# Optimization experiments

Hardware: AMD Instinct MI355X
Metric: run time of the kernel (lower is better)

The kernel has to match this reference:

```python
import jax, jax.numpy as jnp
import numpy as np

NEG_SLOPE = 0.2   # PyG GATConv default leaky_relu slope
L2_EPS = 1e-12    # F.normalize eps


def setup_inputs() -> dict:
    key = jax.random.key(0)
    ks = jax.random.split(key, 10)
    N, E, d = 100000, 600000, 128
    s = 1.0 / np.sqrt(d)
    return {
        "x": jax.random.normal(ks[0], (N, d), jnp.float32),
        "edge_index": jax.random.randint(ks[1], (2, E), 0, N, jnp.int64),
        "W_gat": jax.random.normal(ks[2], (d, d), jnp.float32) * s,
        "att_src": jax.random.normal(ks[3], (d,), jnp.float32) * s,
        "att_dst": jax.random.normal(ks[4], (d,), jnp.float32) * s,
        "b_gat": jax.random.normal(ks[5], (d,), jnp.float32) * s,
        "W_l": jax.random.normal(ks[6], (d, d), jnp.float32) * s,
        "b_l": jax.random.normal(ks[7], (d,), jnp.float32) * s,
        "W_r": jax.random.normal(ks[8], (d, d), jnp.float32) * s,
    }


def reference(x, edge_index, W_gat, att_src, att_dst, b_gat, W_l, b_l, W_r):
    N = x.shape[0]
    src0, dst0 = edge_index[0], edge_index[1]

    # ---- GATConv (heads=1), add_self_loops=True, dropout skipped (eval) ----
    loop = jnp.arange(N, dtype=edge_index.dtype)
    src = jnp.concatenate([src0, loop])
    dst = jnp.concatenate([dst0, loop])

    h = x @ W_gat                           # [N, d]
    a_src = h @ att_src                     # [N]
    a_dst = h @ att_dst                     # [N]
    e = jax.nn.leaky_relu(a_src[src] + a_dst[dst], NEG_SLOPE)  # [E+N]
    # segment softmax over edges sharing the same target node
    m = jax.ops.segment_max(e, dst, num_segments=N)
    p = jnp.exp(e - m[dst])
    z = jax.ops.segment_sum(p, dst, num_segments=N)
    alpha = p / z[dst]
    h_gat = jax.ops.segment_sum(h[src] * alpha[:, None], dst, num_segments=N) + b_gat

    # ---- SAGEConv((x, x_target), edge_index), mean aggr, normalize=True ----
    agg = jax.ops.segment_sum(h_gat[src0], dst0, num_segments=N)   # [N, d]
    cnt = jax.ops.segment_sum(jnp.ones_like(src0, dtype=h_gat.dtype), dst0, num_segments=N)
    mean = agg / jnp.maximum(cnt, 1.0)[:, None]
    out = mean @ W_l + b_l + h_gat @ W_r    # x_target = h_gat[:N]
    # F.normalize(out, p=2, dim=-1)
    norm = jnp.sqrt(jnp.sum(out * out, axis=-1, keepdims=True))
    out = out / jnp.maximum(norm, L2_EPS)
    return out
```

## Files before the change

kernel.cpp:

```cpp
#include <hip/hip_runtime.h>
#include <hip/hip_bf16.h>

#define D 128
#define NEG_SLOPE 0.2f
#define SCAN_BS 512
#define RT 4
#define RTH 2

typedef __attribute__((ext_vector_type(8))) short short8;
typedef __attribute__((ext_vector_type(4))) short short4v;
typedef __attribute__((ext_vector_type(4))) float f32x4;

__device__ __forceinline__ float group_max16(float v) {
#pragma unroll
    for (int m = 8; m >= 1; m >>= 1) v = fmaxf(v, __shfl_xor(v, m));
    return v;
}
__device__ __forceinline__ float group_sum16(float v) {
#pragma unroll
    for (int m = 8; m >= 1; m >>= 1) v += __shfl_xor(v, m);
    return v;
}

__device__ __forceinline__ unsigned short f2bfu(float f) {
    __hip_bfloat16 h = __float2bfloat16(f);
    return *reinterpret_cast<unsigned short*>(&h);
}

__device__ __forceinline__ float bf2f(unsigned short u) {
    return __uint_as_float(((unsigned)u) << 16);
}

__device__ __forceinline__ short8 load_bf8(const float* p) {
    float4 p0 = *(const float4*)p;
    float4 p1 = *(const float4*)(p + 4);
    short8 r;
    r[0] = (short)f2bfu(p0.x); r[1] = (short)f2bfu(p0.y);
    r[2] = (short)f2bfu(p0.z); r[3] = (short)f2bfu(p0.w);
    r[4] = (short)f2bfu(p1.x); r[5] = (short)f2bfu(p1.y);
    r[6] = (short)f2bfu(p1.z); r[7] = (short)f2bfu(p1.w);
    return r;
}

__global__ void k_wt(const float* __restrict__ Wg, const float* __restrict__ Wl,
                     const float* __restrict__ Wr, short* __restrict__ WgT,
                     short* __restrict__ WlT, short* __restrict__ WrT) {
    int i = blockIdx.x * blockDim.x + threadIdx.x;
    int m = i >> 14;
    int r = (i >> 7) & 127;
    int c = i & 127;
    const float* src = (m == 0) ? Wg : (m == 1) ? Wl : Wr;
    short* dst = (m == 0) ? WgT : (m == 1) ? WlT : WrT;
    dst[r * D + c] = (short)f2bfu(src[c * D + r]);
}

__global__ void k_hist(const int* __restrict__ ei, int* __restrict__ cnt, int E) {
    int i = blockIdx.x * blockDim.x + threadIdx.x;
    if (i < E) atomicAdd(&cnt[ei[E + i]], 1);
}

__global__ void k_scan_block(const int* __restrict__ cnt, int* __restrict__ incl,
                             int* __restrict__ btot, int N) {
    __shared__ int s[SCAN_BS];
    int t = threadIdx.x, i = blockIdx.x * SCAN_BS + t;
    int v = (i < N) ? cnt[i] : 0;
    s[t] = v;
    __syncthreads();
    for (int d = 1; d < SCAN_BS; d <<= 1) {
        int u = (t >= d) ? s[t - d] : 0;
        __syncthreads();
        s[t] += u;
        __syncthreads();
    }
    if (i < N) incl[i] = s[t];
    if (t == SCAN_BS - 1) btot[blockIdx.x] = s[t];
}

__global__ void k_scan_tot(int* __restrict__ btot, int nb) {
    __shared__ int s[1024];
    int t = threadIdx.x;
    int v = (t < nb) ? btot[t] : 0;
    s[t] = v;
    __syncthreads();
    for (int d = 1; d < 1024; d <<= 1) {
        int u = (t >= d) ? s[t - d] : 0;
        __syncthreads();
        s[t] += u;
        __syncthreads();
    }
    if (t < nb) btot[t] = s[t] - v;
}

__global__ void k_scan_add(const int* __restrict__ cnt, int* __restrict__ off,
                           const int* __restrict__ btot, int N) {
    int i = blockIdx.x * blockDim.x + threadIdx.x;
    if (i < N) off[i] = off[i] + btot[i / SCAN_BS] - cnt[i];
}

__global__ void k_bucket(const int* __restrict__ ei, const int* __restrict__ off,
                         int* __restrict__ fill, int* __restrict__ csr, int E) {
    int i = blockIdx.x * blockDim.x + threadIdx.x;
    if (i < E) {
        int dt = ei[E + i];
        int p = off[dt] + atomicAdd(&fill[dt], 1);
        csr[p] = ei[i];
    }
}

__global__ void __launch_bounds__(256, 1)
k_gemm_h(const float* __restrict__ x, const short* __restrict__ WgT,
         const float* __restrict__ att_src, const float* __restrict__ att_dst,
         unsigned short* __restrict__ h_bf, float* __restrict__ a_src,
         float* __restrict__ a_dst, int N) {
    __shared__ short lds_w[D * D];
    const int tid = threadIdx.x;
#pragma unroll
    for (int i = 0; i < 8; ++i) {
        int go = (i * 256 + tid) * 16;
        int so = go ^ (((go >> 8) & 7) << 4);
        *(short8*)((char*)lds_w + so) = *(const short8*)((const char*)WgT + go);
    }
    __syncthreads();

    const int lane = tid & 63;
    const int wave = tid >> 6;
    const int lrow = lane & 15, lgrp = lane >> 4;
    const int swz = (lrow & 7) << 4;
    const int base = blockIdx.x * (64 * RTH) + wave * (16 * RTH);

    short8 ax[RTH][4];
    int rows[RTH];
    bool okr[RTH];
#pragma unroll
    for (int t = 0; t < RTH; ++t) {
        rows[t] = base + t * 16 + lrow;
        okr[t] = (rows[t] < N);
        const float* xr = x + (size_t)rows[t] * D + lgrp * 8;
#pragma unroll
        for (int kt = 0; kt < 4; ++kt) {
            if (okr[t]) ax[t][kt] = load_bf8(xr + kt * 32);
            else { short8 zf; for (int j = 0; j < 8; ++j) zf[j] = 0; ax[t][kt] = zf; }
        }
    }

    float ps[RTH], pd[RTH];
#pragma unroll
    for (int t = 0; t < RTH; ++t) { ps[t] = 0.f; pd[t] = 0.f; }

#pragma unroll
    for (int f = 0; f < 8; ++f) {
        short8 wgf[4];
#pragma unroll
        for (int kt = 0; kt < 4; ++kt) {
            int byte = (f * 16 + lrow) * 256 + kt * 64 + lgrp * 16;
            wgf[kt] = *(const short8*)((const char*)lds_w + (byte ^ swz));
        }
        const int cb = f * 16 + lgrp * 4;
        float as[4], adv[4];
#pragma unroll
        for (int j = 0; j < 4; ++j) { as[j] = att_src[cb + j]; adv[j] = att_dst[cb + j]; }
#pragma unroll
        for (int t = 0; t < RTH; ++t) {
            f32x4 a = (f32x4){0.f, 0.f, 0.f, 0.f};
#pragma unroll
            for (int kt = 0; kt < 4; ++kt)
                a = __builtin_amdgcn_mfma_f32_16x16x32_bf16(wgf[kt], ax[t][kt], a, 0, 0, 0);
            short4v hv;
#pragma unroll
            for (int j = 0; j < 4; ++j) {
                float v = a[j];
                hv[j] = (short)f2bfu(v);
                ps[t] += v * as[j];
                pd[t] += v * adv[j];
            }
            if (okr[t]) *(short4v*)(h_bf + (size_t)rows[t] * D + cb) = hv;
        }
    }
#pragma unroll
    for (int t = 0; t < RTH; ++t) {
        float s = ps[t], dd = pd[t];
        s += __shfl_xor(s, 16); s += __shfl_xor(s, 32);
        dd += __shfl_xor(dd, 16); dd += __shfl_xor(dd, 32);
        if (lgrp == 0 && okr[t]) { a_src[rows[t]] = s; a_dst[rows[t]] = dd; }
    }
}

__global__ void k_attn(const int* __restrict__ csr, const int* __restrict__ off,
                       const int* __restrict__ cnt, const float* __restrict__ a_src,
                       const float* __restrict__ a_dst, const unsigned short* __restrict__ h_bf,
                       const float* __restrict__ bg, unsigned short* __restrict__ hg_bf, int N) {
    const int lane = threadIdx.x & 63;
    const int l16 = lane & 15, grp = lane >> 4;
    const int gbase = grp << 4;
    const int d = blockIdx.x * 16 + ((threadIdx.x >> 6) << 2) + grp;
    if (d >= N) return;
    const int deg = cnt[d], o = off[d];
    const float ad = a_dst[d];
    float es = a_src[d] + ad;
    es = (es > 0.f) ? es : NEG_SLOPE * es;

    const int fo = l16 * 8;
    short8 hv = *(const short8*)(h_bf + (size_t)d * D + fo);
    float acc[8];
    float inv;

    if (deg <= 16) {
        int sv = 0;
        float e = -INFINITY;
        if (l16 < deg) {
            sv = csr[o + l16];
            float t = a_src[sv] + ad;
            e = (t > 0.f) ? t : NEG_SLOPE * t;
        }
        float mx = fmaxf(group_max16(e), es);
        float p = (l16 < deg) ? expf(e - mx) : 0.f;
        float pself = expf(es - mx);
        inv = 1.f / (group_sum16(p) + pself);
#pragma unroll
        for (int j = 0; j < 8; ++j) acc[j] = pself * bf2f((unsigned short)hv[j]);
        int i = 0;
        for (; i + 4 <= deg; i += 4) {
            int s0 = __shfl(sv, gbase + i);
            int s1 = __shfl(sv, gbase + i + 1);
            int s2 = __shfl(sv, gbase + i + 2);
            int s3 = __shfl(sv, gbase + i + 3);
            float p0 = __shfl(p, gbase + i);
            float p1 = __shfl(p, gbase + i + 1);
            float p2 = __shfl(p, gbase + i + 2);
            float p3 = __shfl(p, gbase + i + 3);
            short8 r0 = *(const short8*)(h_bf + (size_t)s0 * D + fo);
            short8 r1 = *(const short8*)(h_bf + (size_t)s1 * D + fo);
            short8 r2 = *(const short8*)(h_bf + (size_t)s2 * D + fo);
            short8 r3 = *(const short8*)(h_bf + (size_t)s3 * D + fo);
#pragma unroll
            for (int j = 0; j < 8; ++j)
                acc[j] += p0 * bf2f((unsigned short)r0[j]) + p1 * bf2f((unsigned short)r1[j])
                        + p2 * bf2f((unsigned short)r2[j]) + p3 * bf2f((unsigned short)r3[j]);
        }
        for (; i < deg; ++i) {
            int s = __shfl(sv, gbase + i);
            float pi = __shfl(p, gbase + i);
            short8 row = *(const short8*)(h_bf + (size_t)s * D + fo);
#pragma unroll
            for (int j = 0; j < 8; ++j) acc[j] += pi * bf2f((unsigned short)row[j]);
        }
    } else {
        float m2 = es;
        for (int i = l16; i < deg; i += 16) {
            float t = a_src[csr[o + i]] + ad;
            t = (t > 0.f) ? t : NEG_SLOPE * t;
            m2 = fmaxf(m2, t);
        }
        float mx = group_max16(m2);
        float zp = 0.f;
        for (int i = l16; i < deg; i += 16) {
            float t = a_src[csr[o + i]] + ad;
            t = (t > 0.f) ? t : NEG_SLOPE * t;
            zp += expf(t - mx);
        }
        float pself = expf(es - mx);
        inv = 1.f / (group_sum16(zp) + pself);
#pragma unroll
        for (int j = 0; j < 8; ++j) acc[j] = pself * bf2f((unsigned short)hv[j]);
        for (int i = 0; i < deg; ++i) {
            int s = csr[o + i];
            float t = a_src[s] + ad;
            t = (t > 0.f) ? t : NEG_SLOPE * t;
            float pi = expf(t - mx);
            short8 row = *(const short8*)(h_bf + (size_t)s * D + fo);
#pragma unroll
            for (int j = 0; j < 8; ++j) acc[j] += pi * bf2f((unsigned short)row[j]);
        }
    }
    short8 r;
#pragma unroll
    for (int j = 0; j < 8; ++j) r[j] = (short)f2bfu(acc[j] * inv + bg[fo + j]);
    *(short8*)(hg_bf + (size_t)d * D + fo) = r;
}

__global__ void k_gemm2(const unsigned short* __restrict__ hg_bf,
                        const short* __restrict__ WlT, const short* __restrict__ WrT,
                        unsigned short* __restrict__ hgWl_bf,
                        unsigned short* __restrict__ hgWr_bf, int N) {
    const int lane = threadIdx.x & 63;
    const int wave = threadIdx.x >> 6;
    const int lrow = lane & 15, lgrp = lane >> 4;
    const int base = blockIdx.x * (64 * RT) + wave * (16 * RT);

    short8 ah[RT][4];
    int rows[RT];
    bool okr[RT];
#pragma unroll
    for (int t = 0; t < RT; ++t) {
        rows[t] = base + t * 16 + lrow;
        okr[t] = (rows[t] < N);
        const unsigned short* hp = hg_bf + (size_t)rows[t] * D + lgrp * 8;
#pragma unroll
        for (int kt = 0; kt < 4; ++kt) {
            if (okr[t]) ah[t][kt] = *(const short8*)(hp + kt * 32);
            else { short8 zf; for (int j = 0; j < 8; ++j) zf[j] = 0; ah[t][kt] = zf; }
        }
    }

#pragma unroll
    for (int f = 0; f < 8; ++f) {
        const short* wl = WlT + ((f * 16 + lrow) * D + lgrp * 8);
        const short* wr = WrT + ((f * 16 + lrow) * D + lgrp * 8);
        short8 wlf[4], wrf[4];
#pragma unroll
        for (int kt = 0; kt < 4; ++kt) {
            wlf[kt] = *(const short8*)(wl + kt * 32);
            wrf[kt] = *(const short8*)(wr + kt * 32);
        }
        const int cb = f * 16 + lgrp * 4;
#pragma unroll
        for (int t = 0; t < RT; ++t) {
            f32x4 aL = (f32x4){0.f, 0.f, 0.f, 0.f};
            f32x4 aR = (f32x4){0.f, 0.f, 0.f, 0.f};
#pragma unroll
            for (int kt = 0; kt < 4; ++kt) {
                aL = __builtin_amdgcn_mfma_f32_16x16x32_bf16(wlf[kt], ah[t][kt], aL, 0, 0, 0);
                aR = __builtin_amdgcn_mfma_f32_16x16x32_bf16(wrf[kt], ah[t][kt], aR, 0, 0, 0);
            }
            if (okr[t]) {
                short4v vl, vr;
#pragma unroll
                for (int j = 0; j < 4; ++j) {
                    vl[j] = (short)f2bfu(aL[j]);
                    vr[j] = (short)f2bfu(aR[j]);
                }
                *(short4v*)(hgWl_bf + (size_t)rows[t] * D + cb) = vl;
                *(short4v*)(hgWr_bf + (size_t)rows[t] * D + cb) = vr;
            }
        }
    }
}

__global__ void k_final(const int* __restrict__ csr, const int* __restrict__ off,
                        const int* __restrict__ cnt, const unsigned short* __restrict__ hgWl_bf,
                        const unsigned short* __restrict__ hgWr_bf, const float* __restrict__ bl,
                        float* __restrict__ out, int N) {
    const int lane = threadIdx.x & 63;
    const int l16 = lane & 15, grp = lane >> 4;
    const int gbase = grp << 4;
    const int d = blockIdx.x * 16 + ((threadIdx.x >> 6) << 2) + grp;
    if (d >= N) return;
    const int deg = cnt[d], o = off[d];
    const int fo = l16 * 8;

    short8 wrow = *(const short8*)(hgWr_bf + (size_t)d * D + fo);
    float4 b0 = *(const float4*)(bl + fo);
    float4 b1 = *(const float4*)(bl + fo + 4);

    float acc[8];
#pragma unroll
    for (int j = 0; j < 8; ++j) acc[j] = 0.f;

    if (deg <= 16) {
        int sv = 0;
        if (l16 < deg) sv = csr[o + l16];
        int i = 0;
        for (; i + 4 <= deg; i += 4) {
            int s0 = __shfl(sv, gbase + i);
            int s1 = __shfl(sv, gbase + i + 1);
            int s2 = __shfl(sv, gbase + i + 2);
            int s3 = __shfl(sv, gbase + i + 3);
            short8 r0 = *(const short8*)(hgWl_bf + (size_t)s0 * D + fo);
            short8 r1 = *(const short8*)(hgWl_bf + (size_t)s1 * D + fo);
            short8 r2 = *(const short8*)(hgWl_bf + (size_t)s2 * D + fo);
            short8 r3 = *(const short8*)(hgWl_bf + (size_t)s3 * D + fo);
#pragma unroll
            for (int j = 0; j < 8; ++j)
                acc[j] += bf2f((unsigned short)r0[j]) + bf2f((unsigned short)r1[j])
                        + bf2f((unsigned short)r2[j]) + bf2f((unsigned short)r3[j]);
        }
        for (; i < deg; ++i) {
            int s = __shfl(sv, gbase + i);
            short8 row = *(const short8*)(hgWl_bf + (size_t)s * D + fo);
#pragma unroll
            for (int j = 0; j < 8; ++j) acc[j] += bf2f((unsigned short)row[j]);
        }
    } else {
        for (int i = 0; i < deg; ++i) {
            int s = csr[o + i];
            short8 row = *(const short8*)(hgWl_bf + (size_t)s * D + fo);
#pragma unroll
            for (int j = 0; j < 8; ++j) acc[j] += bf2f((unsigned short)row[j]);
        }
    }

    const float minv = 1.f / fmaxf((float)deg, 1.f);
    float v[8];
    v[0] = acc[0] * minv + bf2f((unsigned short)wrow[0]) + b0.x;
    v[1] = acc[1] * minv + bf2f((unsigned short)wrow[1]) + b0.y;
    v[2] = acc[2] * minv + bf2f((unsigned short)wrow[2]) + b0.z;
    v[3] = acc[3] * minv + bf2f((unsigned short)wrow[3]) + b0.w;
    v[4] = acc[4] * minv + bf2f((unsigned short)wrow[4]) + b1.x;
    v[5] = acc[5] * minv + bf2f((unsigned short)wrow[5]) + b1.y;
    v[6] = acc[6] * minv + bf2f((unsigned short)wrow[6]) + b1.z;
    v[7] = acc[7] * minv + bf2f((unsigned short)wrow[7]) + b1.w;
    float ss = 0.f;
#pragma unroll
    for (int j = 0; j < 8; ++j) ss += v[j] * v[j];
    ss = group_sum16(ss);
    float sc = 1.f / fmaxf(sqrtf(ss), 1e-12f);
    float* orow = out + (size_t)d * D + fo;
    float4 w0 = {v[0] * sc, v[1] * sc, v[2] * sc, v[3] * sc};
    float4 w1 = {v[4] * sc, v[5] * sc, v[6] * sc, v[7] * sc};
    *(float4*)orow = w0;
    *(float4*)(orow + 4) = w1;
}

extern "C" void kernel_launch(void* const* d_in, const int* in_sizes, int n_in,
                              void* d_out, int out_size, void* d_ws, size_t ws_size,
                              hipStream_t stream) {
    const float* x       = (const float*)d_in[0];
    const int*   ei      = (const int*)d_in[1];
    const float* Wg      = (const float*)d_in[2];
    const float* att_src = (const float*)d_in[3];
    const float* att_dst = (const float*)d_in[4];
    const float* bg      = (const float*)d_in[5];
    const float* Wl      = (const float*)d_in[6];
    const float* bl      = (const float*)d_in[7];
    const float* Wr      = (const float*)d_in[8];
    const int N = in_sizes[0] / D;
    const int E = in_sizes[1] / 2;

    char* w = (char*)d_ws;
    unsigned short* h_bf    = (unsigned short*)w;  w += (size_t)N * D * 2;
    unsigned short* hg_bf   = (unsigned short*)w;  w += (size_t)N * D * 2;
    unsigned short* hgWl_bf = (unsigned short*)w;  w += (size_t)N * D * 2;
    unsigned short* hgWr_bf = (unsigned short*)w;  w += (size_t)N * D * 2;
    float* a_src = (float*)w;  w += (size_t)N * 4;
    float* a_dst = (float*)w;  w += (size_t)N * 4;
    int*   cnt_i = (int*)w;    w += (size_t)N * 4;
    int*   off   = (int*)w;    w += (size_t)N * 4;
    int*   fill  = (int*)w;    w += (size_t)N * 4;
    int*   btot  = (int*)w;    w += 1024 * 4;
    int*   csr   = (int*)w;    w += (size_t)E * 4;
    short* WgT   = (short*)w;  w += (size_t)D * D * 2;
    short* WlT   = (short*)w;  w += (size_t)D * D * 2;
    short* WrT   = (short*)w;  w += (size_t)D * D * 2;
    float* out_f = (float*)d_out;

    (void)hipMemsetAsync(cnt_i, 0, (size_t)N * 4, stream);
    (void)hipMemsetAsync(fill, 0, (size_t)N * 4, stream);

    const int nb = (N + SCAN_BS - 1) / SCAN_BS;

    k_wt<<<(3 * D * D) / 256, 256, 0, stream>>>(Wg, Wl, Wr, WgT, WlT, WrT);
    k_hist<<<(E + 255) / 256, 256, 0, stream>>>(ei, cnt_i, E);
    k_scan_block<<<nb, SCAN_BS, 0, stream>>>(cnt_i, off, btot, N);
    k_scan_tot<<<1, 1024, 0, stream>>>(btot, nb);
    k_scan_add<<<(N + 255) / 256, 256, 0, stream>>>(cnt_i, off, btot, N);
    k_bucket<<<(E + 255) / 256, 256, 0, stream>>>(ei, off, fill, csr, E);

    k_gemm_h<<<(N + 64 * RTH - 1) / (64 * RTH), 256, 0, stream>>>(x, WgT, att_src, att_dst, h_bf, a_src, a_dst, N);
    k_attn<<<(N + 15) / 16, 256, 0, stream>>>(csr, off, cnt_i, a_src, a_dst, h_bf, bg, hg_bf, N);
    k_gemm2<<<(N + 64 * RT - 1) / (64 * RT), 256, 0, stream>>>(hg_bf, WlT, WrT, hgWl_bf, hgWr_bf, N);
    k_final<<<(N + 15) / 16, 256, 0, stream>>>(csr, off, cnt_i, hgWl_bf, hgWr_bf, bl, out_f, N);
}
```

Before: 205.4 us.

## Sort destination nodes by degree and drop separate fill counter in CSR build

Adds a counting sort of nodes by in-degree (histogram, scan, scatter into a permutation) so the attention and final aggregation kernels process nodes with similar degree together. This reduces divergence within a wavefront, where the 16-lane groups otherwise take different degree paths. The bucket kernel now bumps off[] atomically instead of using a separate fill array, so the consumers recover the start offset as off - deg, which saves one memset. In exchange it adds three small kernel launches, and the permuted indices break the sequential row locality of the h and output accesses.

```diff
diff --git a/kernel.cpp b/kernel.cpp
--- a/kernel.cpp
+++ b/kernel.cpp
@@ -6,6 +6,7 @@
 #define SCAN_BS 512
 #define RT 4
 #define RTH 2
+#define NBIN 64
 
 typedef __attribute__((ext_vector_type(8))) short short8;
 typedef __attribute__((ext_vector_type(4))) short short4v;
@@ -97,14 +98,51 @@
     if (i < N) off[i] = off[i] + btot[i / SCAN_BS] - cnt[i];
 }
 
-__global__ void k_bucket(const int* __restrict__ ei, const int* __restrict__ off,
-                         int* __restrict__ fill, int* __restrict__ csr, int E) {
+__global__ void k_bucket(const int* __restrict__ ei, int* __restrict__ off,
+                         int* __restrict__ csr, int E) {
     int i = blockIdx.x * blockDim.x + threadIdx.x;
     if (i < E) {
         int dt = ei[E + i];
-        int p = off[dt] + atomicAdd(&fill[dt], 1);
+        int p = atomicAdd(&off[dt], 1);
         csr[p] = ei[i];
     }
+}
+
+__global__ void k_dhist(const int* __restrict__ cnt, int* __restrict__ dbin, int N) {
+    __shared__ int lb[NBIN];
+    int t = threadIdx.x;
+    if (t < NBIN) lb[t] = 0;
+    __syncthreads();
+    int i = blockIdx.x * blockDim.x + t;
+    if (i < N) atomicAdd(&lb[min(cnt[i], NBIN - 1)], 1);
+    __syncthreads();
+    if (t < NBIN && lb[t]) atomicAdd(&dbin[t], lb[t]);
+}
+
+__global__ void k_dscan(const int* __restrict__ dbin, int* __restrict__ dbase) {
+    if (threadIdx.x == 0) {
+        int s = 0;
+        for (int b = 0; b < NBIN; ++b) { dbase[b] = s; s += dbin[b]; }
+    }
+}
+
+__global__ void k_dscat(const int* __restrict__ cnt, const int* __restrict__ dbase,
+                        int* __restrict__ dfill, int* __restrict__ perm, int N) {
+    __shared__ int lb[NBIN];
+    __shared__ int gb[NBIN];
+    int t = threadIdx.x;
+    if (t < NBIN) lb[t] = 0;
+    __syncthreads();
+    int i = blockIdx.x * blockDim.x + t;
+    int b = 0, lr = 0;
+    if (i < N) {
+        b = min(cnt[i], NBIN - 1);
+        lr = atomicAdd(&lb[b], 1);
+    }
+    __syncthreads();
+    if (t < NBIN) gb[t] = lb[t] ? atomicAdd(&dfill[t], lb[t]) : 0;
+    __syncthreads();
+    if (i < N) perm[dbase[b] + gb[b] + lr] = i;
 }
 
 __global__ void __launch_bounds__(256, 1)
@@ -185,16 +223,19 @@
     }
 }
 
-__global__ void k_attn(const int* __restrict__ csr, const int* __restrict__ off,
-                       const int* __restrict__ cnt, const float* __restrict__ a_src,
-                       const float* __restrict__ a_dst, const unsigned short* __restrict__ h_bf,
-                       const float* __restrict__ bg, unsigned short* __restrict__ hg_bf, int N) {
+__global__ void k_attn(const int* __restrict__ perm, const int* __restrict__ csr,
+                       const int* __restrict__ off, const int* __restrict__ cnt,
+                       const float* __restrict__ a_src, const float* __restrict__ a_dst,
+                       const unsigned short* __restrict__ h_bf, const float* __restrict__ bg,
+                       unsigned short* __restrict__ hg_bf, int N) {
     const int lane = threadIdx.x & 63;
     const int l16 = lane & 15, grp = lane >> 4;
     const int gbase = grp << 4;
-    const int d = blockIdx.x * 16 + ((threadIdx.x >> 6) << 2) + grp;
-    if (d >= N) return;
-    const int deg = cnt[d], o = off[d];
+    const int idx = blockIdx.x * 16 + ((threadIdx.x >> 6) << 2) + grp;
+    if (idx >= N) return;
+    const int d = perm[idx];
+    const int deg = cnt[d];
+    const int o = off[d] - deg;
     const float ad = a_dst[d];
     float es = a_src[d] + ad;
     es = (es > 0.f) ? es : NEG_SLOPE * es;
@@ -336,16 +377,19 @@
     }
 }
 
-__global__ void k_final(const int* __restrict__ csr, const int* __restrict__ off,
-                        const int* __restrict__ cnt, const unsigned short* __restrict__ hgWl_bf,
+__global__ void k_final(const int* __restrict__ perm, const int* __restrict__ csr,
+                        const int* __restrict__ off, const int* __restrict__ cnt,
+                        const unsigned short* __restrict__ hgWl_bf,
                         const unsigned short* __restrict__ hgWr_bf, const float* __restrict__ bl,
                         float* __restrict__ out, int N) {
     const int lane = threadIdx.x & 63;
     const int l16 = lane & 15, grp = lane >> 4;
     const int gbase = grp << 4;
-    const int d = blockIdx.x * 16 + ((threadIdx.x >> 6) << 2) + grp;
-    if (d >= N) return;
-    const int deg = cnt[d], o = off[d];
+    const int idx = blockIdx.x * 16 + ((threadIdx.x >> 6) << 2) + grp;
+    if (idx >= N) return;
+    const int d = perm[idx];
+    const int deg = cnt[d];
+    const int o = off[d] - deg;
     const int fo = l16 * 8;
 
     short8 wrow = *(const short8*)(hgWr_bf + (size_t)d * D + fo);
@@ -435,8 +479,11 @@
     float* a_dst = (float*)w;  w += (size_t)N * 4;
     int*   cnt_i = (int*)w;    w += (size_t)N * 4;
     int*   off   = (int*)w;    w += (size_t)N * 4;
-    int*   fill  = (int*)w;    w += (size_t)N * 4;
+    int*   perm  = (int*)w;    w += (size_t)N * 4;
     int*   btot  = (int*)w;    w += 1024 * 4;
+    int*   dbin  = (int*)w;    w += NBIN * 4;
+    int*   dbase = (int*)w;    w += NBIN * 4;
+    int*   dfill = (int*)w;    w += NBIN * 4;
     int*   csr   = (int*)w;    w += (size_t)E * 4;
     short* WgT   = (short*)w;  w += (size_t)D * D * 2;
     short* WlT   = (short*)w;  w += (size_t)D * D * 2;
@@ -444,7 +491,7 @@
     float* out_f = (float*)d_out;
 
     (void)hipMemsetAsync(cnt_i, 0, (size_t)N * 4, stream);
-    (void)hipMemsetAsync(fill, 0, (size_t)N * 4, stream);
+    (void)hipMemsetAsync(dbin, 0, (size_t)3 * NBIN * 4, stream);
 
     const int nb = (N + SCAN_BS - 1) / SCAN_BS;
 
@@ -453,10 +500,13 @@
     k_scan_block<<<nb, SCAN_BS, 0, stream>>>(cnt_i, off, btot, N);
     k_scan_tot<<<1, 1024, 0, stream>>>(btot, nb);
     k_scan_add<<<(N + 255) / 256, 256, 0, stream>>>(cnt_i, off, btot, N);
-    k_bucket<<<(E + 255) / 256, 256, 0, stream>>>(ei, off, fill, csr, E);
+    k_bucket<<<(E + 255) / 256, 256, 0, stream>>>(ei, off, csr, E);
+    k_dhist<<<(N + 255) / 256, 256, 0, stream>>>(cnt_i, dbin, N);
+    k_dscan<<<1, 64, 0, stream>>>(dbin, dbase);
+    k_dscat<<<(N + 255) / 256, 256, 0, stream>>>(cnt_i, dbase, dfill, perm, N);
 
     k_gemm_h<<<(N + 64 * RTH - 1) / (64 * RTH), 256, 0, stream>>>(x, WgT, att_src, att_dst, h_bf, a_src, a_dst, N);
-    k_attn<<<(N + 15) / 16, 256, 0, stream>>>(csr, off, cnt_i, a_src, a_dst, h_bf, bg, hg_bf, N);
+    k_attn<<<(N + 15) / 16, 256, 0, stream>>>(perm, csr, off, cnt_i, a_src, a_dst, h_bf, bg, hg_bf, N);
     k_gemm2<<<(N + 64 * RT - 1) / (64 * RT), 256, 0, stream>>>(hg_bf, WlT, WrT, hgWl_bf, hgWr_bf, N);
-    k_final<<<(N + 15) / 16, 256, 0, stream>>>(csr, off, cnt_i, hgWl_bf, hgWr_bf, bl, out_f, N);
-}
+    k_final<<<(N + 15) / 16, 256, 0, stream>>>(perm, csr, off, cnt_i, hgWl_bf, hgWr_bf, bl, out_f, N);
+}
```

Result: slower. 235.1 us (+14.5%).
